# Kernel tuning notes

Hardware: AMD Instinct MI355X
Metric: run time of the kernel (lower is better)

Reference implementation:

```python
import jax, jax.numpy as jnp
import numpy as np

B, D, E, H, O, K = 8192, 3072, 8, 2048, 512, 2
EPS = float(np.finfo(float).eps)  # np.finfo(float).eps used in SparseDispatcher.combine


def _cv_squared(v):
    # torch .var() is unbiased (ddof=1)
    v = v.astype(jnp.float32)
    return jnp.var(v, ddof=1) / (jnp.mean(v) ** 2 + 1e-10)


def setup_inputs() -> dict:
    key = jax.random.key(0)
    ks = jax.random.split(key, 8)
    x = jax.random.normal(ks[0], (B, D), dtype=jnp.float32)
    Cats = jax.random.uniform(ks[1], (B, E), dtype=jnp.float32)
    w_gate = jax.random.normal(ks[2], (D, E), dtype=jnp.float32) * 0.01
    # per-expert 2-layer MLP standing in for the per-expert ResNet
    W1 = jax.random.normal(ks[3], (E, D, H), dtype=jnp.float32) * (1.0 / np.sqrt(D))
    b1 = jnp.zeros((E, H), dtype=jnp.float32)
    W2 = jax.random.normal(ks[4], (E, H, O), dtype=jnp.float32) * (1.0 / np.sqrt(H))
    b2 = jnp.zeros((E, O), dtype=jnp.float32)
    return {"x": x, "Cats": Cats, "w_gate": w_gate, "W1": W1, "b1": b1,
            "W2": W2, "b2": b2, "train": 0}


def reference(x, Cats, w_gate, W1, b1, W2, b2, train):
    # ---- top_k_gating (eval path; train branch mutates optimizer state) ----
    logits = x @ w_gate                                   # [B, E]
    top_vals, top_idx = jax.lax.top_k(logits, min(K + 1, E))
    top_k_vals = top_vals[:, :K]                          # [B, K]
    top_k_idx = top_idx[:, :K]                            # [B, K]
    top_k_gates = jax.nn.softmax(top_k_vals, axis=1)      # softmax over kept logits
    rows = jnp.arange(x.shape[0])[:, None]
    gates = jnp.zeros_like(logits).at[rows, top_k_idx].set(top_k_gates)  # scatter

    load = (gates > 0).sum(axis=0)                        # tokens per expert
    importance = gates.sum(axis=0)
    aux_loss = 0.01 * (_cv_squared(importance) + _cv_squared(load))

    # ---- dispatch / expert / combine ----
    # Dense grouped form: expert_i runs on its routed tokens; tokens with
    # gates[b,i]==0 contribute exactly 0 to the combine, identical math to
    # SparseDispatcher's gather/split + exp*gate + index_add + log.
    h = jax.nn.relu(jnp.einsum('bd,edh->beh', x, W1) + b1[None])  # [B, E, H]
    out = jnp.einsum('beh,eho->beo', h, W2) + b2[None]            # [B, E, O]
    combined = jnp.einsum('be,beo->bo', gates, jnp.exp(out))      # exp, *gate, sum
    combined = jnp.where(combined == 0, EPS, combined)
    y = jnp.log(combined)
    return (y, aux_loss)
```

## Files before the change

### kernel.cpp

```cpp
#include <hip/hip_runtime.h>
#include <stdint.h>


typedef __bf16 bf16x8 __attribute__((ext_vector_type(8)));
typedef __bf16 bf16x4 __attribute__((ext_vector_type(4)));
typedef float floatx4 __attribute__((ext_vector_type(4)));

#define EPSF 2.2204460492503131e-16f

__device__ __forceinline__ void gl_lds16(const void* g, void* l) {
  __builtin_amdgcn_global_load_lds(
      (__attribute__((address_space(1))) void*)(g),
      (__attribute__((address_space(3))) void*)(l), 16, 0, 0);
}

__global__ __launch_bounds__(512) void k_gating(
    const float* __restrict__ x, const float* __restrict__ wg,
    __bf16* __restrict__ x_bf, int* __restrict__ expsel,
    float* __restrict__ gpair) {
  __shared__ float wgs[12320];
  const int tid = threadIdx.x;
  const int lane = tid & 63;
  const int w = tid >> 6;
  const int r = blockIdx.x * 8 + w;
  const int g = lane >> 3;
  const int e = lane & 7;
  const float* xr = x + (size_t)r * 3072;
  __bf16* xbr = x_bf + (size_t)r * 3072;

#pragma unroll
  for (int t = 0; t < 12; ++t) {
    const int d = t * 256 + lane * 4;
    const float4 xv = *(const float4*)(xr + d);
    bf16x4 xo;
    xo.x = (__bf16)xv.x; xo.y = (__bf16)xv.y;
    xo.z = (__bf16)xv.z; xo.w = (__bf16)xv.w;
    *(bf16x4*)(xbr + d) = xo;
  }

  double a0 = 0.0, a1 = 0.0;
  for (int h = 0; h < 2; ++h) {
    __syncthreads();
#pragma unroll
    for (int t = 0; t < 6; ++t) {
      const int wi = t * 2048 + tid * 4;
      const int gg = wi / 1536;
      const float4 v = *(const float4*)(wg + h * 12288 + wi);
      *(float4*)(wgs + wi + 4 * gg) = v;
    }
    __syncthreads();
    const float* xrg = xr + h * 1536 + g * 192;
    const float* wbase = wgs + g * 1540 + e;
    for (int i = 0; i < 192; i += 4) {
      const float4 xv = *(const float4*)(xrg + i);
      a0 += (double)xv.x * (double)wbase[(i + 0) * 8];
      a1 += (double)xv.y * (double)wbase[(i + 1) * 8];
      a0 += (double)xv.z * (double)wbase[(i + 2) * 8];
      a1 += (double)xv.w * (double)wbase[(i + 3) * 8];
    }
  }
  double v = a0 + a1;
  v += __shfl_xor(v, 8);
  v += __shfl_xor(v, 16);
  v += __shfl_xor(v, 32);
  double le[8];
#pragma unroll
  for (int ee = 0; ee < 8; ++ee) le[ee] = __shfl(v, ee);
  if (lane == 0) {
    int i0 = 0; double v0 = le[0];
#pragma unroll
    for (int k = 1; k < 8; ++k) if (le[k] > v0) { v0 = le[k]; i0 = k; }
    int i1 = (i0 == 0) ? 1 : 0; double v1 = le[i1];
#pragma unroll
    for (int k = 0; k < 8; ++k)
      if (k != i0 && le[k] > v1 && k != i1) { v1 = le[k]; i1 = k; }
    const float tt = (float)exp(v1 - v0);
    const float g0 = 1.0f / (1.0f + tt);
    const float g1 = tt / (1.0f + tt);
    expsel[r] = i0 | (i1 << 4);
    gpair[r * 2] = g0;
    gpair[r * 2 + 1] = g1;
  }
}

__global__ __launch_bounds__(256) void k_build_lists(
    const int* __restrict__ expsel, const float* __restrict__ gpair,
    int* __restrict__ lists, int* __restrict__ cnt, double* __restrict__ imp) {
  const int e = blockIdx.x;
  const int tid = threadIdx.x;
  const int lane = tid & 63;
  const int w = tid >> 6;
  __shared__ int wsum[4];
  __shared__ double dsum[4];
  int base = 0;
  double gsum = 0.0;
  int* out = lists + e * 8192;
  for (int c = 0; c < 32; ++c) {
    const int r = c * 256 + tid;
    const int sel = expsel[r];
    const bool m0 = ((sel & 15) == e);
    const bool m1 = (((sel >> 4) & 15) == e);
    const bool m = m0 || m1;
    const int entry = 2 * r + (m1 ? 1 : 0);
    const unsigned long long mask = __ballot(m);
    const int wcount = __popcll(mask);
    const int pos = __popcll(mask & ((1ull << lane) - 1ull));
    if (lane == 0) wsum[w] = wcount;
    __syncthreads();
    int pre = base;
#pragma unroll
    for (int ww = 0; ww < 4; ++ww) if (ww < w) pre += wsum[ww];
    const int total = wsum[0] + wsum[1] + wsum[2] + wsum[3];
    if (m) {
      out[pre + pos] = entry;
      gsum += (double)gpair[entry];
    }
    base += total;
    __syncthreads();
  }
  gsum += __shfl_down(gsum, 32);
  gsum += __shfl_down(gsum, 16);
  gsum += __shfl_down(gsum, 8);
  gsum += __shfl_down(gsum, 4);
  gsum += __shfl_down(gsum, 2);
  gsum += __shfl_down(gsum, 1);
  if (lane == 0) dsum[w] = gsum;
  __syncthreads();
  if (tid == 0) {
    imp[e] = dsum[0] + dsum[1] + dsum[2] + dsum[3];
    cnt[e] = base;
  }
}

__global__ void k_sched_aux(const int* __restrict__ cnt, const double* __restrict__ imp,
                            int* __restrict__ sched, int* __restrict__ nslots,
                            float* __restrict__ aux_out) {
  if (threadIdx.x != 0 || blockIdx.x != 0) return;
  int ns = 0;
  for (int e = 0; e < 8; ++e) {
    const int c = cnt[e];
    const int t = (c + 127) >> 7;
    for (int i = 0; i < t; ++i) { sched[2 * ns] = e; sched[2 * ns + 1] = i << 7; ++ns; }
  }
  *nslots = ns;
  double mi = 0.0, ml = 0.0;
  for (int e = 0; e < 8; ++e) { mi += imp[e]; ml += (double)cnt[e]; }
  mi *= 0.125; ml *= 0.125;
  double vi = 0.0, vl = 0.0;
  for (int e = 0; e < 8; ++e) {
    const double di = imp[e] - mi; vi += di * di;
    const double dl = (double)cnt[e] - ml; vl += dl * dl;
  }
  vi /= 7.0; vl /= 7.0;
  aux_out[0] = (float)(0.01 * (vi / (mi * mi + 1e-10) + vl / (ml * ml + 1e-10)));
}

__global__ __launch_bounds__(256) void k_transpose_cvt(
    const float* __restrict__ in, __bf16* __restrict__ out, int R, int C) {
  __shared__ float tile[64][65];
  const int e = blockIdx.z;
  const int c0 = blockIdx.x * 64;
  const int r0 = blockIdx.y * 64;
  const float* src = in + (size_t)e * R * C + (size_t)r0 * C + c0;
  __bf16* dst = out + (size_t)e * R * C + (size_t)c0 * R + r0;
  const int tx = threadIdx.x & 15;
  const int ty = threadIdx.x >> 4;
#pragma unroll
  for (int i = 0; i < 4; ++i) {
    const int row = ty + i * 16;
    const float4 v = *(const float4*)(src + (size_t)row * C + tx * 4);
    tile[row][tx * 4 + 0] = v.x;
    tile[row][tx * 4 + 1] = v.y;
    tile[row][tx * 4 + 2] = v.z;
    tile[row][tx * 4 + 3] = v.w;
  }
  __syncthreads();
#pragma unroll
  for (int i = 0; i < 4; ++i) {
    const int cc = ty + i * 16;
    const int rr = tx * 4;
    bf16x4 o;
    o.x = (__bf16)tile[rr + 0][cc];
    o.y = (__bf16)tile[rr + 1][cc];
    o.z = (__bf16)tile[rr + 2][cc];
    o.w = (__bf16)tile[rr + 3][cc];
    *(bf16x4*)(dst + (size_t)cc * R + rr) = o;
  }
}

template <int KDIM, int MODE>
__global__ __launch_bounds__(256, 2) void k_moe_gemm(
    const __bf16* __restrict__ Asrc, const __bf16* __restrict__ Ball,
    const float* __restrict__ bias, const int* __restrict__ lists,
    const int* __restrict__ cnt, const int* __restrict__ sched,
    const int* __restrict__ nslots, const float* __restrict__ gpair,
    __bf16* __restrict__ hout, float* __restrict__ oout) {
  constexpr int NDIM = (MODE == 0) ? 2048 : 512;
  const int slot = blockIdx.y;
  if (slot >= *nslots) return;
  const int e = sched[2 * slot];
  const int row0 = sched[2 * slot + 1];
  const int cnte = cnt[e];
  const int n0 = blockIdx.x * 128;

  __shared__ unsigned short As[128 * 32];
  __shared__ unsigned short Bs[128 * 32];

  const int tid = threadIdx.x;
  const int lane = tid & 63;
  const int wid = __builtin_amdgcn_readfirstlane(tid >> 6);
  const int wm = wid >> 1;
  const int wn = wid & 1;

  const __bf16* Be = Ball + (size_t)e * NDIM * KDIM;
  const int* liste = lists + e * 8192;
  const int acol = (lane & 3) * 8;

  const __bf16* aptr[2];
  const __bf16* bptr[2];
#pragma unroll
  for (int p = 0; p < 2; ++p) {
    const int chunk = wid + 4 * p;
    const int lr = chunk * 16 + (lane >> 2);
    int m = row0 + lr;
    m = (m < cnte) ? m : (cnte - 1);
    const int entry = liste[m];
    const int srow = (MODE == 0) ? (entry >> 1) : entry;
    aptr[p] = Asrc + (size_t)srow * KDIM + acol;
    bptr[p] = Be + (size_t)(n0 + lr) * KDIM + acol;
  }

  floatx4 acc[4][4];
#pragma unroll
  for (int i = 0; i < 4; ++i)
#pragma unroll
    for (int j = 0; j < 4; ++j) {
      acc[i][j].x = 0.f; acc[i][j].y = 0.f; acc[i][j].z = 0.f; acc[i][j].w = 0.f;
    }

  for (int k0 = 0; k0 < KDIM; k0 += 32) {
#pragma unroll
    for (int p = 0; p < 2; ++p) {
      gl_lds16(aptr[p] + k0, &As[(wid + 4 * p) * 512]);
      gl_lds16(bptr[p] + k0, &Bs[(wid + 4 * p) * 512]);
    }
    __syncthreads();
    bf16x8 af[4], bfr[4];
    const int rdoff = (lane & 15) * 32 + (lane >> 4) * 8;
#pragma unroll
    for (int i = 0; i < 4; ++i)
      af[i] = *(const bf16x8*)&As[(wm * 64 + i * 16) * 32 + rdoff];
#pragma unroll
    for (int j = 0; j < 4; ++j)
      bfr[j] = *(const bf16x8*)&Bs[(wn * 64 + j * 16) * 32 + rdoff];
    __syncthreads();
#pragma unroll
    for (int i = 0; i < 4; ++i)
#pragma unroll
      for (int j = 0; j < 4; ++j)
        acc[i][j] = __builtin_amdgcn_mfma_f32_16x16x32_bf16(af[i], bfr[j], acc[i][j], 0, 0, 0);
  }

  const int cq = lane >> 4;
  const int cn = lane & 15;
#pragma unroll
  for (int i = 0; i < 4; ++i) {
#pragma unroll
    for (int r = 0; r < 4; ++r) {
      const int m = row0 + wm * 64 + i * 16 + cq * 4 + r;
      if (m < cnte) {
        const int p = liste[m];
        if (MODE == 0) {
          __bf16* orow = hout + (size_t)p * 2048;
#pragma unroll
          for (int j = 0; j < 4; ++j) {
            const int n = n0 + wn * 64 + j * 16 + cn;
            float v = acc[i][j][r] + bias[e * 2048 + n];
            v = v > 0.0f ? v : 0.0f;
            orow[n] = (__bf16)v;
          }
        } else {
          float* orow = oout + (size_t)p * 512;
          const float g = gpair[p];
#pragma unroll
          for (int j = 0; j < 4; ++j) {
            const int n = n0 + wn * 64 + j * 16 + cn;
            const float v = acc[i][j][r] + bias[e * 512 + n];
            orow[n] = g * __expf(v);
          }
        }
      }
    }
  }
}

__global__ __launch_bounds__(128) void k_combine(const float* __restrict__ op,
                                                 float* __restrict__ y) {
  const int r = blockIdx.x;
  const int o = threadIdx.x * 4;
  const float4 a = *(const float4*)(op + (size_t)(2 * r) * 512 + o);
  const float4 b = *(const float4*)(op + (size_t)(2 * r + 1) * 512 + o);
  float4 res;
  float s;
  s = a.x + b.x; if (s == 0.0f) s = EPSF; res.x = logf(s);
  s = a.y + b.y; if (s == 0.0f) s = EPSF; res.y = logf(s);
  s = a.z + b.z; if (s == 0.0f) s = EPSF; res.z = logf(s);
  s = a.w + b.w; if (s == 0.0f) s = EPSF; res.w = logf(s);
  *(float4*)(y + (size_t)r * 512 + o) = res;
}

extern "C" void kernel_launch(void* const* d_in, const int* in_sizes, int n_in,
                              void* d_out, int out_size, void* d_ws, size_t ws_size,
                              hipStream_t stream) {
  (void)in_sizes; (void)n_in; (void)out_size; (void)ws_size;
  const float* x  = (const float*)d_in[0];
  const float* wg = (const float*)d_in[2];
  const float* W1 = (const float*)d_in[3];
  const float* b1 = (const float*)d_in[4];
  const float* W2 = (const float*)d_in[5];
  const float* b2 = (const float*)d_in[6];
  float* y = (float*)d_out;

  char* w = (char*)d_ws;
  __bf16* x_bf = (__bf16*)w; w += (size_t)8192 * 3072 * 2;
  __bf16* w1t  = (__bf16*)w; w += (size_t)8 * 2048 * 3072 * 2;
  __bf16* w2t  = (__bf16*)w; w += (size_t)8 * 512 * 2048 * 2;
  __bf16* hp   = (__bf16*)w; w += (size_t)16384 * 2048 * 2;
  float*  op   = (float*)w;  w += (size_t)16384 * 512 * 4;
  int*    lists= (int*)w;    w += (size_t)8 * 8192 * 4;
  float*  gpr  = (float*)w;  w += (size_t)16384 * 4;
  int*    expsel=(int*)w;    w += (size_t)8192 * 4;
  int*    cnt  = (int*)w;    w += 64;
  double* imp  = (double*)w; w += 64;
  int*    sched= (int*)w;    w += 2 * 136 * 4;
  int*    nslots=(int*)w;    w += 64;

  hipLaunchKernelGGL(k_gating, dim3(1024), dim3(512), 0, stream, x, wg, x_bf, expsel, gpr);
  hipLaunchKernelGGL(k_build_lists, dim3(8), dim3(256), 0, stream, expsel, gpr, lists, cnt, imp);
  hipLaunchKernelGGL(k_transpose_cvt, dim3(32, 48, 8), dim3(256), 0, stream, W1, w1t, 3072, 2048);
  hipLaunchKernelGGL(k_transpose_cvt, dim3(8, 32, 8), dim3(256), 0, stream, W2, w2t, 2048, 512);
  hipLaunchKernelGGL(k_sched_aux, dim3(1), dim3(64), 0, stream, cnt, imp, sched, nslots,
                     y + (size_t)8192 * 512);
  hipLaunchKernelGGL((k_moe_gemm<3072, 0>), dim3(16, 136), dim3(256), 0, stream,
                     x_bf, w1t, b1, lists, cnt, sched, nslots, (const float*)nullptr,
                     hp, (float*)nullptr);
  hipLaunchKernelGGL((k_moe_gemm<2048, 1>), dim3(4, 136), dim3(256), 0, stream,
                     hp, w2t, b2, lists, cnt, sched, nslots, gpr,
                     (__bf16*)nullptr, op);
  hipLaunchKernelGGL(k_combine, dim3(8192), dim3(128), 0, stream, op, y);
}
```

Before: 804.3 us.

## Double K-step per sync, shrink second GEMM N-tile, swap grid order

The grouped MoE GEMM now loads a 64-deep K slice per iteration instead of 32, which halves the number of barrier pairs per tile. The second GEMM uses a 64-wide N tile, giving more blocks for the smaller output. The grid is reordered so consecutive blocks walk over row slots for the same N tile, which may improve weight reuse in L2. The larger LDS footprint (up to 32KB) and the higher launch bound of 3 blocks per CU could raise register pressure or cause spills.

```diff
diff --git a/kernel.cpp b/kernel.cpp
--- a/kernel.cpp
+++ b/kernel.cpp
@@ -189,22 +189,25 @@
 }
 
 template <int KDIM, int MODE>
-__global__ __launch_bounds__(256, 2) void k_moe_gemm(
+__global__ __launch_bounds__(256, 3) void k_moe_gemm(
     const __bf16* __restrict__ Asrc, const __bf16* __restrict__ Ball,
     const float* __restrict__ bias, const int* __restrict__ lists,
     const int* __restrict__ cnt, const int* __restrict__ sched,
     const int* __restrict__ nslots, const float* __restrict__ gpair,
     __bf16* __restrict__ hout, float* __restrict__ oout) {
   constexpr int NDIM = (MODE == 0) ? 2048 : 512;
-  const int slot = blockIdx.y;
+  constexpr int BN = (MODE == 0) ? 128 : 64;
+  constexpr int BPASS = BN / 32;
+  constexpr int NJ = BN / 32;
+  const int slot = blockIdx.x;
   if (slot >= *nslots) return;
   const int e = sched[2 * slot];
   const int row0 = sched[2 * slot + 1];
   const int cnte = cnt[e];
-  const int n0 = blockIdx.x * 128;
-
-  __shared__ unsigned short As[128 * 32];
-  __shared__ unsigned short Bs[128 * 32];
+  const int n0 = blockIdx.y * BN;
+
+  __shared__ unsigned short As[128 * 64];
+  __shared__ unsigned short Bs[BN * 64];
 
   const int tid = threadIdx.x;
   const int lane = tid & 63;
@@ -214,51 +217,58 @@
 
   const __bf16* Be = Ball + (size_t)e * NDIM * KDIM;
   const int* liste = lists + e * 8192;
-  const int acol = (lane & 3) * 8;
-
-  const __bf16* aptr[2];
-  const __bf16* bptr[2];
-#pragma unroll
-  for (int p = 0; p < 2; ++p) {
-    const int chunk = wid + 4 * p;
-    const int lr = chunk * 16 + (lane >> 2);
+  const int c8 = (lane & 7) * 8;
+
+  const __bf16* aptr[4];
+#pragma unroll
+  for (int p = 0; p < 4; ++p) {
+    const int lr = p * 32 + wid * 8 + (lane >> 3);
     int m = row0 + lr;
     m = (m < cnte) ? m : (cnte - 1);
     const int entry = liste[m];
     const int srow = (MODE == 0) ? (entry >> 1) : entry;
-    aptr[p] = Asrc + (size_t)srow * KDIM + acol;
-    bptr[p] = Be + (size_t)(n0 + lr) * KDIM + acol;
-  }
-
-  floatx4 acc[4][4];
+    aptr[p] = Asrc + (size_t)srow * KDIM + c8;
+  }
+  const __bf16* bptr[BPASS];
+#pragma unroll
+  for (int q = 0; q < BPASS; ++q) {
+    const int lr = q * 32 + wid * 8 + (lane >> 3);
+    bptr[q] = Be + (size_t)(n0 + lr) * KDIM + c8;
+  }
+
+  floatx4 acc[4][NJ];
 #pragma unroll
   for (int i = 0; i < 4; ++i)
 #pragma unroll
-    for (int j = 0; j < 4; ++j) {
+    for (int j = 0; j < NJ; ++j) {
       acc[i][j].x = 0.f; acc[i][j].y = 0.f; acc[i][j].z = 0.f; acc[i][j].w = 0.f;
     }
 
-  for (int k0 = 0; k0 < KDIM; k0 += 32) {
-#pragma unroll
-    for (int p = 0; p < 2; ++p) {
-      gl_lds16(aptr[p] + k0, &As[(wid + 4 * p) * 512]);
-      gl_lds16(bptr[p] + k0, &Bs[(wid + 4 * p) * 512]);
-    }
-    __syncthreads();
-    bf16x8 af[4], bfr[4];
-    const int rdoff = (lane & 15) * 32 + (lane >> 4) * 8;
-#pragma unroll
-    for (int i = 0; i < 4; ++i)
-      af[i] = *(const bf16x8*)&As[(wm * 64 + i * 16) * 32 + rdoff];
-#pragma unroll
-    for (int j = 0; j < 4; ++j)
-      bfr[j] = *(const bf16x8*)&Bs[(wn * 64 + j * 16) * 32 + rdoff];
-    __syncthreads();
-#pragma unroll
-    for (int i = 0; i < 4; ++i)
-#pragma unroll
-      for (int j = 0; j < 4; ++j)
-        acc[i][j] = __builtin_amdgcn_mfma_f32_16x16x32_bf16(af[i], bfr[j], acc[i][j], 0, 0, 0);
+  for (int k0 = 0; k0 < KDIM; k0 += 64) {
+#pragma unroll
+    for (int p = 0; p < 4; ++p)
+      gl_lds16(aptr[p] + k0, &As[p * 2048 + wid * 512]);
+#pragma unroll
+    for (int q = 0; q < BPASS; ++q)
+      gl_lds16(bptr[q] + k0, &Bs[q * 2048 + wid * 512]);
+    __syncthreads();
+    const int rbase = (lane & 15) * 64 + (lane >> 4) * 8;
+#pragma unroll
+    for (int s = 0; s < 2; ++s) {
+      bf16x8 af[4], bfr[NJ];
+#pragma unroll
+      for (int i = 0; i < 4; ++i)
+        af[i] = *(const bf16x8*)&As[(wm * 64 + i * 16) * 64 + s * 32 + rbase];
+#pragma unroll
+      for (int j = 0; j < NJ; ++j)
+        bfr[j] = *(const bf16x8*)&Bs[(wn * (NJ * 16) + j * 16) * 64 + s * 32 + rbase];
+#pragma unroll
+      for (int i = 0; i < 4; ++i)
+#pragma unroll
+        for (int j = 0; j < NJ; ++j)
+          acc[i][j] = __builtin_amdgcn_mfma_f32_16x16x32_bf16(af[i], bfr[j], acc[i][j], 0, 0, 0);
+    }
+    __syncthreads();
   }
 
   const int cq = lane >> 4;
@@ -273,8 +283,8 @@
         if (MODE == 0) {
           __bf16* orow = hout + (size_t)p * 2048;
 #pragma unroll
-          for (int j = 0; j < 4; ++j) {
-            const int n = n0 + wn * 64 + j * 16 + cn;
+          for (int j = 0; j < NJ; ++j) {
+            const int n = n0 + wn * (NJ * 16) + j * 16 + cn;
             float v = acc[i][j][r] + bias[e * 2048 + n];
             v = v > 0.0f ? v : 0.0f;
             orow[n] = (__bf16)v;
@@ -283,8 +293,8 @@
           float* orow = oout + (size_t)p * 512;
           const float g = gpair[p];
 #pragma unroll
-          for (int j = 0; j < 4; ++j) {
-            const int n = n0 + wn * 64 + j * 16 + cn;
+          for (int j = 0; j < NJ; ++j) {
+            const int n = n0 + wn * (NJ * 16) + j * 16 + cn;
             const float v = acc[i][j][r] + bias[e * 512 + n];
             orow[n] = g * __expf(v);
           }
@@ -341,10 +351,10 @@
   hipLaunchKernelGGL(k_transpose_cvt, dim3(8, 32, 8), dim3(256), 0, stream, W2, w2t, 2048, 512);
   hipLaunchKernelGGL(k_sched_aux, dim3(1), dim3(64), 0, stream, cnt, imp, sched, nslots,
                      y + (size_t)8192 * 512);
-  hipLaunchKernelGGL((k_moe_gemm<3072, 0>), dim3(16, 136), dim3(256), 0, stream,
+  hipLaunchKernelGGL((k_moe_gemm<3072, 0>), dim3(136, 16), dim3(256), 0, stream,
                      x_bf, w1t, b1, lists, cnt, sched, nslots, (const float*)nullptr,
                      hp, (float*)nullptr);
-  hipLaunchKernelGGL((k_moe_gemm<2048, 1>), dim3(4, 136), dim3(256), 0, stream,
+  hipLaunchKernelGGL((k_moe_gemm<2048, 1>), dim3(136, 8), dim3(256), 0, stream,
                      hp, w2t, b2, lists, cnt, sched, nslots, gpr,
                      (__bf16*)nullptr, op);
   hipLaunchKernelGGL(k_combine, dim3(8192), dim3(128), 0, stream, op, y);
```

Result: slower. 842.0 us (+4.7%).
